# Kernel tuning notes

Hardware: AMD Instinct MI355X
Metric: run time of the kernel (lower is better)

## Reference

```python
import jax, jax.numpy as jnp
import numpy as np

DT = 1e-4  # integration step, matches Model(dt=0.0001)
T = 4_000_000


def setup_inputs() -> dict:
    key = jax.random.key(0)
    ks = jax.random.split(key, 8)
    inputs = jax.random.normal(ks[0], (1, T, 3), dtype=jnp.float32)
    # time column made increasing (as in a real signal record)
    t = jnp.arange(T, dtype=jnp.float32) * DT
    inputs = inputs.at[0, :, 0].set(t)
    # small-scale 2x2 system matrices; A shifted toward -0.5*I so the
    # 4M-step linear recurrence is stable (no overflow over long horizons)
    A = -0.5 * jnp.eye(2, dtype=jnp.float32) + 0.05 * jax.random.normal(ks[1], (2, 2), jnp.float32)
    B = 0.1 * jax.random.normal(ks[2], (2, 2), jnp.float32)
    D = 0.1 * jax.random.normal(ks[3], (2, 2), jnp.float32)
    E = 0.1 * jax.random.normal(ks[4], (2, 2), jnp.float32)
    cov_in = 0.1 * jax.random.normal(ks[5], (2, 2), jnp.float32)
    training_params = jax.random.normal(ks[6], (1, 2), jnp.float32)
    initial_states = jnp.zeros((1, 5), dtype=jnp.float32)
    return {"inputs": inputs, "A": A, "B": B, "D": D, "E": E,
            "cov_in": cov_in, "training_params": training_params,
            "initial_states": initial_states}


def reference(inputs, A, B, D, E, cov_in, training_params, initial_states):
    # Faithful to GRCell.call: cov = cov_in every step (new_cov is discarded),
    # so XiCov / XiCovC / transition matrix are time-invariant constants.
    dt = jnp.float32(DT)
    sqrt2 = jnp.sqrt(jnp.float32(2.0))
    x_signal = jnp.array([1.0, 0.0], dtype=inputs.dtype)
    XiCov = (E - cov_in @ B) / sqrt2                      # (2,2)
    XiCovC = XiCov @ (-sqrt2 * B.T)                       # (2,2)
    Trans = jnp.eye(2, dtype=inputs.dtype) + (A - XiCovC) * dt  # I + (A-XiCovC)dt
    Cout = -sqrt2 * B.T * dt                              # output map, (2,2)
    p0 = training_params[0, 0]
    p1 = training_params[0, 1]
    seq = inputs[0]                                       # [T, 3] = (time, dy1, dy2)

    def step(x, inp):
        t = inp[0]
        dy = inp[1:]
        out = Cout @ x                                    # emitted BEFORE update
        x_new = Trans @ x + XiCov @ dy + (p0 * jnp.cos(p1 * t) * dt) * x_signal
        return x_new, out

    x0 = initial_states[0, :2]
    _, outs = jax.lax.scan(step, x0, seq)                 # outs: [T, 2]
    return outs[None]                                     # [1, T, 2]
```

## Files before the change

kernel.cpp:

```cpp
#include <hip/hip_runtime.h>
#include <math.h>


constexpr int   TN    = 4000000;
constexpr float FDT   = 1e-4f;
constexpr int   L     = 16;
constexpr int   LOG2L = 4;
constexpr int   K     = TN / L;
constexpr int   BT    = 256;
constexpr int   NB    = (K + BT - 1) / BT;
constexpr int   ROW   = 13;
constexpr int   F4IN  = TN * 3 / 4;
constexpr int   F4OUT = TN * 2 / 4;

struct Consts {
  float T00, T01, T10, T11;
  float X00, X01, X10, X11;
  float C00, C01, C10, C11;
  float p0, p1;
};

__device__ inline Consts make_consts(const float* __restrict__ A,
                                     const float* __restrict__ B,
                                     const float* __restrict__ E,
                                     const float* __restrict__ cov,
                                     const float* __restrict__ tp) {
  const float s2 = 1.41421356237309515f;
  Consts c;
  float Xi[2][2];
  for (int i = 0; i < 2; ++i)
    for (int j = 0; j < 2; ++j)
      Xi[i][j] = (E[i*2+j] - (cov[i*2+0]*B[0*2+j] + cov[i*2+1]*B[1*2+j])) / s2;
  float XiC[2][2];
  for (int i = 0; i < 2; ++i)
    for (int j = 0; j < 2; ++j)
      XiC[i][j] = Xi[i][0]*(-s2*B[j*2+0]) + Xi[i][1]*(-s2*B[j*2+1]);
  c.T00 = 1.0f + (A[0] - XiC[0][0]) * FDT;
  c.T01 =        (A[1] - XiC[0][1]) * FDT;
  c.T10 =        (A[2] - XiC[1][0]) * FDT;
  c.T11 = 1.0f + (A[3] - XiC[1][1]) * FDT;
  c.X00 = Xi[0][0]; c.X01 = Xi[0][1]; c.X10 = Xi[1][0]; c.X11 = Xi[1][1];
  c.C00 = -s2 * B[0] * FDT;
  c.C01 = -s2 * B[2] * FDT;
  c.C10 = -s2 * B[1] * FDT;
  c.C11 = -s2 * B[3] * FDT;
  c.p0 = tp[0]; c.p1 = tp[1];
  return c;
}

__device__ inline void step(float& x0, float& x1, float t, float a, float b,
                            const Consts& c) {
  float u0 = fmaf(c.X00, a, fmaf(c.X01, b, c.p0 * __cosf(c.p1 * t) * FDT));
  float u1 = fmaf(c.X10, a, c.X11 * b);
  float n0 = fmaf(c.T00, x0, fmaf(c.T01, x1, u0));
  float n1 = fmaf(c.T10, x0, fmaf(c.T11, x1, u1));
  x0 = n0; x1 = n1;
}

__device__ inline void dsq(double* M) {
  double a = M[0]*M[0] + M[1]*M[2];
  double b = M[0]*M[1] + M[1]*M[3];
  double d = M[2]*M[0] + M[3]*M[2];
  double e = M[2]*M[1] + M[3]*M[3];
  M[0] = a; M[1] = b; M[2] = d; M[3] = e;
}

__device__ inline void dmm(const double* a, const double* b, double* o) {
  o[0] = a[0]*b[0] + a[1]*b[2];
  o[1] = a[0]*b[1] + a[1]*b[3];
  o[2] = a[2]*b[0] + a[3]*b[2];
  o[3] = a[2]*b[1] + a[3]*b[3];
}

__device__ inline void pow_table(const Consts& c, double (*Pw)[4], int n) {
  double M[4] = {(double)c.T00, (double)c.T01, (double)c.T10, (double)c.T11};
  for (int s = 0; s < LOG2L; ++s) dsq(M);
  Pw[0][0] = M[0]; Pw[0][1] = M[1]; Pw[0][2] = M[2]; Pw[0][3] = M[3];
  for (int i = 1; i < n; ++i) {
    dsq(M);
    Pw[i][0] = M[0]; Pw[i][1] = M[1]; Pw[i][2] = M[2]; Pw[i][3] = M[3];
  }
}

__global__ void __launch_bounds__(BT)
k1(const float* __restrict__ seq, const float* __restrict__ A,
   const float* __restrict__ B, const float* __restrict__ E,
   const float* __restrict__ cov, const float* __restrict__ tp,
   float2* __restrict__ Xe, double2* __restrict__ agg) {
  __shared__ float4  ls[BT * ROW];
  __shared__ double  wg[4][2];
  const int tid  = threadIdx.x;
  const int lane = tid & 63;
  const int w    = tid >> 6;
  const int k    = blockIdx.x * BT + tid;
  Consts c = make_consts(A, B, E, cov, tp);

  const float4* seq4 = (const float4*)seq;
  const size_t base = (size_t)blockIdx.x * (BT * 12);
  #pragma unroll
  for (int i = 0; i < 12; ++i) {
    int lf = i * BT + tid;
    size_t f = base + (size_t)lf;
    float4 v = make_float4(0.f, 0.f, 0.f, 0.f);
    if (f < (size_t)F4IN) v = seq4[f];
    int cc = lf / 12, s = lf - cc * 12;
    ls[cc * ROW + s] = v;
  }
  __syncthreads();

  float x0 = 0.f, x1 = 0.f;
  const float4* row = &ls[tid * ROW];
  #pragma unroll
  for (int q = 0; q < 4; ++q) {
    float4 fa = row[3*q], fb = row[3*q+1], fc = row[3*q+2];
    step(x0, x1, fa.x, fa.y, fa.z, c);
    step(x0, x1, fa.w, fb.x, fb.y, c);
    step(x0, x1, fb.z, fb.w, fc.x, c);
    step(x0, x1, fc.y, fc.z, fc.w, c);
  }

  double Pw[7][4];
  pow_table(c, Pw, 7);

  double v0 = (double)x0, v1 = (double)x1;
  #pragma unroll
  for (int s = 0; s < 6; ++s) {
    int st = 1 << s;
    double p0 = __shfl_up(v0, st);
    double p1 = __shfl_up(v1, st);
    if (lane >= st) {
      double n0 = Pw[s][0]*p0 + Pw[s][1]*p1 + v0;
      double n1 = Pw[s][2]*p0 + Pw[s][3]*p1 + v1;
      v0 = n0; v1 = n1;
    }
  }
  if (lane == 63) { wg[w][0] = v0; wg[w][1] = v1; }
  __syncthreads();

  double E0 = 0.0, E1 = 0.0;
  for (int ww = 0; ww < w; ++ww) {
    double n0 = Pw[6][0]*E0 + Pw[6][1]*E1 + wg[ww][0];
    double n1 = Pw[6][2]*E0 + Pw[6][3]*E1 + wg[ww][1];
    E0 = n0; E1 = n1;
  }

  double pv0 = __shfl_up(v0, 1);
  double pv1 = __shfl_up(v1, 1);
  if (lane == 0) { pv0 = 0.0; pv1 = 0.0; }

  double M0 = 1.0, M1 = 0.0, M2 = 0.0, M3 = 1.0;
  #pragma unroll
  for (int b = 0; b < 6; ++b) {
    if ((lane >> b) & 1) {
      double a0 = Pw[b][0]*M0 + Pw[b][1]*M2;
      double a1 = Pw[b][0]*M1 + Pw[b][1]*M3;
      double a2 = Pw[b][2]*M0 + Pw[b][3]*M2;
      double a3 = Pw[b][2]*M1 + Pw[b][3]*M3;
      M0 = a0; M1 = a1; M2 = a2; M3 = a3;
    }
  }
  double e0 = M0*E0 + M1*E1 + pv0;
  double e1 = M2*E0 + M3*E1 + pv1;
  if (k < K) Xe[k] = make_float2((float)e0, (float)e1);
  if (tid == BT - 1) {
    double a0 = Pw[6][0]*E0 + Pw[6][1]*E1 + v0;
    double a1 = Pw[6][2]*E0 + Pw[6][3]*E1 + v1;
    agg[blockIdx.x] = make_double2(a0, a1);
  }
}

__global__ void __launch_bounds__(BT)
k2(const float* __restrict__ A, const float* __restrict__ B,
   const float* __restrict__ E, const float* __restrict__ cov,
   const float* __restrict__ tp, const float* __restrict__ ini,
   const double2* __restrict__ agg, double2* __restrict__ Yb) {
  __shared__ double wg[4][2];
  const int tid = threadIdx.x, lane = tid & 63, w = tid >> 6;
  Consts c = make_consts(A, B, E, cov, tp);

  double Q[4] = {(double)c.T00, (double)c.T01, (double)c.T10, (double)c.T11};
  for (int s = 0; s < LOG2L + 8; ++s) dsq(Q);
  double Q2[4], Q3[4], Q4[4];
  dmm(Q, Q, Q2); dmm(Q2, Q, Q3); dmm(Q2, Q2, Q4);
  double QW[7][4];
  for (int i = 0; i < 4; ++i) QW[0][i] = Q4[i];
  for (int s = 1; s < 7; ++s) dmm(QW[s-1], QW[s-1], QW[s]);

  double i0 = 0.0, i1 = 0.0;
  double inc[4][2];
  #pragma unroll
  for (int j = 0; j < 4; ++j) {
    int idx = 4 * tid + j;
    double e0 = 0.0, e1 = 0.0;
    if (idx == 0)      { e0 = (double)ini[0]; e1 = (double)ini[1]; }
    else if (idx < NB) { double2 a = agg[idx-1]; e0 = a.x; e1 = a.y; }
    double n0 = Q[0]*i0 + Q[1]*i1 + e0;
    double n1 = Q[2]*i0 + Q[3]*i1 + e1;
    i0 = n0; i1 = n1;
    inc[j][0] = i0; inc[j][1] = i1;
  }

  double v0 = i0, v1 = i1;
  #pragma unroll
  for (int s = 0; s < 6; ++s) {
    int st = 1 << s;
    double p0 = __shfl_up(v0, st);
    double p1 = __shfl_up(v1, st);
    if (lane >= st) {
      double n0 = QW[s][0]*p0 + QW[s][1]*p1 + v0;
      double n1 = QW[s][2]*p0 + QW[s][3]*p1 + v1;
      v0 = n0; v1 = n1;
    }
  }
  if (lane == 63) { wg[w][0] = v0; wg[w][1] = v1; }
  __syncthreads();
  double E0 = 0.0, E1 = 0.0;
  for (int ww = 0; ww < w; ++ww) {
    double n0 = QW[6][0]*E0 + QW[6][1]*E1 + wg[ww][0];
    double n1 = QW[6][2]*E0 + QW[6][3]*E1 + wg[ww][1];
    E0 = n0; E1 = n1;
  }
  double pv0 = __shfl_up(v0, 1);
  double pv1 = __shfl_up(v1, 1);
  if (lane == 0) { pv0 = 0.0; pv1 = 0.0; }

  double M0 = 1.0, M1 = 0.0, M2 = 0.0, M3 = 1.0;
  #pragma unroll
  for (int b = 0; b < 6; ++b) {
    if ((lane >> b) & 1) {
      double a0 = QW[b][0]*M0 + QW[b][1]*M2;
      double a1 = QW[b][0]*M1 + QW[b][1]*M3;
      double a2 = QW[b][2]*M0 + QW[b][3]*M2;
      double a3 = QW[b][2]*M1 + QW[b][3]*M3;
      M0 = a0; M1 = a1; M2 = a2; M3 = a3;
    }
  }
  double Eth0 = M0*E0 + M1*E1 + pv0;
  double Eth1 = M2*E0 + M3*E1 + pv1;

  const double* Pj[4] = {Q, Q2, Q3, Q4};
  #pragma unroll
  for (int j = 0; j < 4; ++j) {
    int idx = 4 * tid + j;
    if (idx < NB) {
      double y0 = Pj[j][0]*Eth0 + Pj[j][1]*Eth1 + inc[j][0];
      double y1 = Pj[j][2]*Eth0 + Pj[j][3]*Eth1 + inc[j][1];
      Yb[idx] = make_double2(y0, y1);
    }
  }
}

__global__ void __launch_bounds__(BT)
k3(const float* __restrict__ seq, const float* __restrict__ A,
   const float* __restrict__ B, const float* __restrict__ E,
   const float* __restrict__ cov, const float* __restrict__ tp,
   const float2* __restrict__ Xe, const double2* __restrict__ Yb,
   float* __restrict__ out) {
  __shared__ float4 ls[BT * ROW];
  const int tid = threadIdx.x;
  const int k   = blockIdx.x * BT + tid;
  Consts c = make_consts(A, B, E, cov, tp);

  const float4* seq4 = (const float4*)seq;
  const size_t base = (size_t)blockIdx.x * (BT * 12);
  #pragma unroll
  for (int i = 0; i < 12; ++i) {
    int lf = i * BT + tid;
    size_t f = base + (size_t)lf;
    float4 v = make_float4(0.f, 0.f, 0.f, 0.f);
    if (f < (size_t)F4IN) v = seq4[f];
    int cc = lf / 12, s = lf - cc * 12;
    ls[cc * ROW + s] = v;
  }
  __syncthreads();

  double Pw[8][4];
  pow_table(c, Pw, 8);
  double M0 = 1.0, M1 = 0.0, M2 = 0.0, M3 = 1.0;
  #pragma unroll
  for (int b = 0; b < 8; ++b) {
    if ((tid >> b) & 1) {
      double a0 = Pw[b][0]*M0 + Pw[b][1]*M2;
      double a1 = Pw[b][0]*M1 + Pw[b][1]*M3;
      double a2 = Pw[b][2]*M0 + Pw[b][3]*M2;
      double a3 = Pw[b][2]*M1 + Pw[b][3]*M3;
      M0 = a0; M1 = a1; M2 = a2; M3 = a3;
    }
  }
  double2 yb = Yb[blockIdx.x];
  float2 xe = (k < K) ? Xe[k] : make_float2(0.f, 0.f);
  float x0 = (float)(M0*yb.x + M1*yb.y + (double)xe.x);
  float x1 = (float)(M2*yb.x + M3*yb.y + (double)xe.y);

  float4* row = &ls[tid * ROW];
  #pragma unroll
  for (int q = 0; q < 4; ++q) {
    float4 fa = row[3*q], fb = row[3*q+1], fc = row[3*q+2];
    float4 oA, oB;
    oA.x = fmaf(c.C00, x0, c.C01 * x1); oA.y = fmaf(c.C10, x0, c.C11 * x1);
    step(x0, x1, fa.x, fa.y, fa.z, c);
    oA.z = fmaf(c.C00, x0, c.C01 * x1); oA.w = fmaf(c.C10, x0, c.C11 * x1);
    step(x0, x1, fa.w, fb.x, fb.y, c);
    oB.x = fmaf(c.C00, x0, c.C01 * x1); oB.y = fmaf(c.C10, x0, c.C11 * x1);
    step(x0, x1, fb.z, fb.w, fc.x, c);
    oB.z = fmaf(c.C00, x0, c.C01 * x1); oB.w = fmaf(c.C10, x0, c.C11 * x1);
    step(x0, x1, fc.y, fc.z, fc.w, c);
    row[2*q]   = oA;
    row[2*q+1] = oB;
  }
  __syncthreads();

  float4* out4 = (float4*)out;
  const size_t obase = (size_t)blockIdx.x * (BT * 8);
  #pragma unroll
  for (int i = 0; i < 8; ++i) {
    int lf = i * BT + tid;
    size_t g = obase + (size_t)lf;
    if (g < (size_t)F4OUT) {
      int cc = lf >> 3, s = lf & 7;
      out4[g] = ls[cc * ROW + s];
    }
  }
}

extern "C" void kernel_launch(void* const* d_in, const int* in_sizes, int n_in,
                              void* d_out, int out_size, void* d_ws, size_t ws_size,
                              hipStream_t stream) {
  const float* seq = (const float*)d_in[0];
  const float* A   = (const float*)d_in[1];
  const float* B   = (const float*)d_in[2];
  const float* E   = (const float*)d_in[4];
  const float* cov = (const float*)d_in[5];
  const float* tp  = (const float*)d_in[6];
  const float* ini = (const float*)d_in[7];
  float* out = (float*)d_out;

  float2*  Xe  = (float2*)d_ws;
  double2* agg = (double2*)((char*)d_ws + 2000000);
  double2* Yb  = (double2*)((char*)d_ws + 2000000 + 16384);

  k1<<<NB, BT, 0, stream>>>(seq, A, B, E, cov, tp, Xe, agg);
  k2<<<1,  BT, 0, stream>>>(A, B, E, cov, tp, ini, agg, Yb);
  k3<<<NB, BT, 0, stream>>>(seq, A, B, E, cov, tp, Xe, Yb, out);
}
```

Baseline: 127.0 us.

## Fuse three scan kernels into one persistent kernel with grid barrier

The three launches (local scan, block-carry scan, fixup) become one persistent kernel of 512 blocks, each handling up to two tiles. An atomic grid barrier separates the phases, and every block redundantly computes the cross-block carry scan. Per-thread carries stay in registers, so the Xe/Yb workspace round trips and two launch gaps go away. The cost is a spin barrier that assumes all 512 blocks are co-resident, a memset launch, and reloading the inputs from global memory in the second phase.

Result: slower. 356.5 us (+180.8%).

```diff
diff --git a/kernel.cpp b/kernel.cpp
--- a/kernel.cpp
+++ b/kernel.cpp
@@ -8,7 +8,8 @@
 constexpr int   LOG2L = 4;
 constexpr int   K     = TN / L;
 constexpr int   BT    = 256;
-constexpr int   NB    = (K + BT - 1) / BT;
+constexpr int   NT    = (K + BT - 1) / BT;
+constexpr int   NBLK  = 512;
 constexpr int   ROW   = 13;
 constexpr int   F4IN  = TN * 3 / 4;
 constexpr int   F4OUT = TN * 2 / 4;
@@ -72,114 +73,127 @@
   o[3] = a[2]*b[1] + a[3]*b[3];
 }
 
-__device__ inline void pow_table(const Consts& c, double (*Pw)[4], int n) {
+__device__ inline void mulleft(const double* P, double* M) {
+  double a0 = P[0]*M[0] + P[1]*M[2];
+  double a1 = P[0]*M[1] + P[1]*M[3];
+  double a2 = P[2]*M[0] + P[3]*M[2];
+  double a3 = P[2]*M[1] + P[3]*M[3];
+  M[0]=a0; M[1]=a1; M[2]=a2; M[3]=a3;
+}
+
+__device__ inline void pow_table(const Consts& c, double (*Pt)[4], int n) {
   double M[4] = {(double)c.T00, (double)c.T01, (double)c.T10, (double)c.T11};
   for (int s = 0; s < LOG2L; ++s) dsq(M);
-  Pw[0][0] = M[0]; Pw[0][1] = M[1]; Pw[0][2] = M[2]; Pw[0][3] = M[3];
+  Pt[0][0] = M[0]; Pt[0][1] = M[1]; Pt[0][2] = M[2]; Pt[0][3] = M[3];
   for (int i = 1; i < n; ++i) {
     dsq(M);
-    Pw[i][0] = M[0]; Pw[i][1] = M[1]; Pw[i][2] = M[2]; Pw[i][3] = M[3];
-  }
-}
-
-__global__ void __launch_bounds__(BT)
-k1(const float* __restrict__ seq, const float* __restrict__ A,
-   const float* __restrict__ B, const float* __restrict__ E,
-   const float* __restrict__ cov, const float* __restrict__ tp,
-   float2* __restrict__ Xe, double2* __restrict__ agg) {
-  __shared__ float4  ls[BT * ROW];
-  __shared__ double  wg[4][2];
+    Pt[i][0] = M[0]; Pt[i][1] = M[1]; Pt[i][2] = M[2]; Pt[i][3] = M[3];
+  }
+}
+
+__global__ void __launch_bounds__(BT, 2)
+fused(const float* __restrict__ seq, const float* __restrict__ A,
+      const float* __restrict__ B, const float* __restrict__ Em,
+      const float* __restrict__ cov, const float* __restrict__ tp,
+      const float* __restrict__ ini,
+      int* __restrict__ bar, double* __restrict__ agg,
+      float* __restrict__ out) {
+  __shared__ float4 ls[BT * ROW];
+  __shared__ double wg[4][2];
+  __shared__ double sY[2][2];
   const int tid  = threadIdx.x;
   const int lane = tid & 63;
   const int w    = tid >> 6;
-  const int k    = blockIdx.x * BT + tid;
-  Consts c = make_consts(A, B, E, cov, tp);
+  const int bid  = blockIdx.x;
+  Consts c = make_consts(A, B, Em, cov, tp);
+
+  double Pt[8][4];
+  pow_table(c, Pt, 8);
+
+  double Mt[4] = {1,0,0,1};
+  #pragma unroll
+  for (int b = 0; b < 8; ++b) if ((tid >> b) & 1) mulleft(Pt[b], Mt);
+  double Ml[4] = {1,0,0,1};
+  #pragma unroll
+  for (int b = 0; b < 6; ++b) if ((lane >> b) & 1) mulleft(Pt[b], Ml);
 
   const float4* seq4 = (const float4*)seq;
-  const size_t base = (size_t)blockIdx.x * (BT * 12);
-  #pragma unroll
-  for (int i = 0; i < 12; ++i) {
-    int lf = i * BT + tid;
-    size_t f = base + (size_t)lf;
-    float4 v = make_float4(0.f, 0.f, 0.f, 0.f);
-    if (f < (size_t)F4IN) v = seq4[f];
-    int cc = lf / 12, s = lf - cc * 12;
-    ls[cc * ROW + s] = v;
-  }
+  double xe[2][2];
+
+  for (int tt = 0; tt < 2; ++tt) {
+    int t = bid + tt * NBLK;
+    if (t >= NT) break;
+    if (tt) __syncthreads();
+    const size_t base = (size_t)t * (BT * 12);
+    #pragma unroll
+    for (int i = 0; i < 12; ++i) {
+      int lf = i * BT + tid;
+      size_t f = base + (size_t)lf;
+      float4 v = make_float4(0.f, 0.f, 0.f, 0.f);
+      if (f < (size_t)F4IN) v = seq4[f];
+      int cc = lf / 12, s = lf - cc * 12;
+      ls[cc * ROW + s] = v;
+    }
+    __syncthreads();
+
+    float x0 = 0.f, x1 = 0.f;
+    const float4* row = &ls[tid * ROW];
+    #pragma unroll
+    for (int q = 0; q < 4; ++q) {
+      float4 fa = row[3*q], fb = row[3*q+1], fc = row[3*q+2];
+      step(x0, x1, fa.x, fa.y, fa.z, c);
+      step(x0, x1, fa.w, fb.x, fb.y, c);
+      step(x0, x1, fb.z, fb.w, fc.x, c);
+      step(x0, x1, fc.y, fc.z, fc.w, c);
+    }
+
+    double v0 = (double)x0, v1 = (double)x1;
+    #pragma unroll
+    for (int s = 0; s < 6; ++s) {
+      int st = 1 << s;
+      double p0 = __shfl_up(v0, st);
+      double p1 = __shfl_up(v1, st);
+      if (lane >= st) {
+        double n0 = Pt[s][0]*p0 + Pt[s][1]*p1 + v0;
+        double n1 = Pt[s][2]*p0 + Pt[s][3]*p1 + v1;
+        v0 = n0; v1 = n1;
+      }
+    }
+    if (lane == 63) { wg[w][0] = v0; wg[w][1] = v1; }
+    __syncthreads();
+    double E0 = 0.0, E1 = 0.0;
+    for (int ww = 0; ww < w; ++ww) {
+      double n0 = Pt[6][0]*E0 + Pt[6][1]*E1 + wg[ww][0];
+      double n1 = Pt[6][2]*E0 + Pt[6][3]*E1 + wg[ww][1];
+      E0 = n0; E1 = n1;
+    }
+    double pv0 = __shfl_up(v0, 1);
+    double pv1 = __shfl_up(v1, 1);
+    if (lane == 0) { pv0 = 0.0; pv1 = 0.0; }
+    xe[tt][0] = Ml[0]*E0 + Ml[1]*E1 + pv0;
+    xe[tt][1] = Ml[2]*E0 + Ml[3]*E1 + pv1;
+    if (tid == BT - 1) {
+      double a0 = Pt[6][0]*E0 + Pt[6][1]*E1 + v0;
+      double a1 = Pt[6][2]*E0 + Pt[6][3]*E1 + v1;
+      __hip_atomic_store(&agg[2*t],   a0, __ATOMIC_RELEASE, __HIP_MEMORY_SCOPE_AGENT);
+      __hip_atomic_store(&agg[2*t+1], a1, __ATOMIC_RELEASE, __HIP_MEMORY_SCOPE_AGENT);
+    }
+  }
+
+  __threadfence();
   __syncthreads();
-
-  float x0 = 0.f, x1 = 0.f;
-  const float4* row = &ls[tid * ROW];
-  #pragma unroll
-  for (int q = 0; q < 4; ++q) {
-    float4 fa = row[3*q], fb = row[3*q+1], fc = row[3*q+2];
-    step(x0, x1, fa.x, fa.y, fa.z, c);
-    step(x0, x1, fa.w, fb.x, fb.y, c);
-    step(x0, x1, fb.z, fb.w, fc.x, c);
-    step(x0, x1, fc.y, fc.z, fc.w, c);
-  }
-
-  double Pw[7][4];
-  pow_table(c, Pw, 7);
-
-  double v0 = (double)x0, v1 = (double)x1;
-  #pragma unroll
-  for (int s = 0; s < 6; ++s) {
-    int st = 1 << s;
-    double p0 = __shfl_up(v0, st);
-    double p1 = __shfl_up(v1, st);
-    if (lane >= st) {
-      double n0 = Pw[s][0]*p0 + Pw[s][1]*p1 + v0;
-      double n1 = Pw[s][2]*p0 + Pw[s][3]*p1 + v1;
-      v0 = n0; v1 = n1;
-    }
-  }
-  if (lane == 63) { wg[w][0] = v0; wg[w][1] = v1; }
+  if (tid == 0) {
+    __hip_atomic_fetch_add(bar, 1, __ATOMIC_ACQ_REL, __HIP_MEMORY_SCOPE_AGENT);
+    long guard = 0;
+    while (__hip_atomic_load(bar, __ATOMIC_ACQUIRE, __HIP_MEMORY_SCOPE_AGENT) < NBLK) {
+      __builtin_amdgcn_s_sleep(2);
+      if (++guard > (1L << 26)) break;
+    }
+  }
   __syncthreads();
 
-  double E0 = 0.0, E1 = 0.0;
-  for (int ww = 0; ww < w; ++ww) {
-    double n0 = Pw[6][0]*E0 + Pw[6][1]*E1 + wg[ww][0];
-    double n1 = Pw[6][2]*E0 + Pw[6][3]*E1 + wg[ww][1];
-    E0 = n0; E1 = n1;
-  }
-
-  double pv0 = __shfl_up(v0, 1);
-  double pv1 = __shfl_up(v1, 1);
-  if (lane == 0) { pv0 = 0.0; pv1 = 0.0; }
-
-  double M0 = 1.0, M1 = 0.0, M2 = 0.0, M3 = 1.0;
-  #pragma unroll
-  for (int b = 0; b < 6; ++b) {
-    if ((lane >> b) & 1) {
-      double a0 = Pw[b][0]*M0 + Pw[b][1]*M2;
-      double a1 = Pw[b][0]*M1 + Pw[b][1]*M3;
-      double a2 = Pw[b][2]*M0 + Pw[b][3]*M2;
-      double a3 = Pw[b][2]*M1 + Pw[b][3]*M3;
-      M0 = a0; M1 = a1; M2 = a2; M3 = a3;
-    }
-  }
-  double e0 = M0*E0 + M1*E1 + pv0;
-  double e1 = M2*E0 + M3*E1 + pv1;
-  if (k < K) Xe[k] = make_float2((float)e0, (float)e1);
-  if (tid == BT - 1) {
-    double a0 = Pw[6][0]*E0 + Pw[6][1]*E1 + v0;
-    double a1 = Pw[6][2]*E0 + Pw[6][3]*E1 + v1;
-    agg[blockIdx.x] = make_double2(a0, a1);
-  }
-}
-
-__global__ void __launch_bounds__(BT)
-k2(const float* __restrict__ A, const float* __restrict__ B,
-   const float* __restrict__ E, const float* __restrict__ cov,
-   const float* __restrict__ tp, const float* __restrict__ ini,
-   const double2* __restrict__ agg, double2* __restrict__ Yb) {
-  __shared__ double wg[4][2];
-  const int tid = threadIdx.x, lane = tid & 63, w = tid >> 6;
-  Consts c = make_consts(A, B, E, cov, tp);
-
-  double Q[4] = {(double)c.T00, (double)c.T01, (double)c.T10, (double)c.T11};
-  for (int s = 0; s < LOG2L + 8; ++s) dsq(Q);
+  double Q[4] = {Pt[7][0], Pt[7][1], Pt[7][2], Pt[7][3]};
+  dsq(Q);
   double Q2[4], Q3[4], Q4[4];
   dmm(Q, Q, Q2); dmm(Q2, Q, Q3); dmm(Q2, Q2, Q4);
   double QW[7][4];
@@ -192,14 +206,16 @@
   for (int j = 0; j < 4; ++j) {
     int idx = 4 * tid + j;
     double e0 = 0.0, e1 = 0.0;
-    if (idx == 0)      { e0 = (double)ini[0]; e1 = (double)ini[1]; }
-    else if (idx < NB) { double2 a = agg[idx-1]; e0 = a.x; e1 = a.y; }
+    if (idx == 0) { e0 = (double)ini[0]; e1 = (double)ini[1]; }
+    else if (idx < NT) {
+      e0 = __hip_atomic_load(&agg[2*(idx-1)],   __ATOMIC_ACQUIRE, __HIP_MEMORY_SCOPE_AGENT);
+      e1 = __hip_atomic_load(&agg[2*(idx-1)+1], __ATOMIC_ACQUIRE, __HIP_MEMORY_SCOPE_AGENT);
+    }
     double n0 = Q[0]*i0 + Q[1]*i1 + e0;
     double n1 = Q[2]*i0 + Q[3]*i1 + e1;
     i0 = n0; i1 = n1;
     inc[j][0] = i0; inc[j][1] = i1;
   }
-
   double v0 = i0, v1 = i1;
   #pragma unroll
   for (int s = 0; s < 6; ++s) {
@@ -223,7 +239,6 @@
   double pv0 = __shfl_up(v0, 1);
   double pv1 = __shfl_up(v1, 1);
   if (lane == 0) { pv0 = 0.0; pv1 = 0.0; }
-
   double M0 = 1.0, M1 = 0.0, M2 = 0.0, M3 = 1.0;
   #pragma unroll
   for (int b = 0; b < 6; ++b) {
@@ -238,87 +253,66 @@
   double Eth0 = M0*E0 + M1*E1 + pv0;
   double Eth1 = M2*E0 + M3*E1 + pv1;
 
-  const double* Pj[4] = {Q, Q2, Q3, Q4};
-  #pragma unroll
-  for (int j = 0; j < 4; ++j) {
-    int idx = 4 * tid + j;
-    if (idx < NB) {
+  {
+    const double* Pj[4] = {Q, Q2, Q3, Q4};
+    #pragma unroll
+    for (int j = 0; j < 4; ++j) {
+      int idx = 4 * tid + j;
       double y0 = Pj[j][0]*Eth0 + Pj[j][1]*Eth1 + inc[j][0];
       double y1 = Pj[j][2]*Eth0 + Pj[j][3]*Eth1 + inc[j][1];
-      Yb[idx] = make_double2(y0, y1);
-    }
-  }
-}
-
-__global__ void __launch_bounds__(BT)
-k3(const float* __restrict__ seq, const float* __restrict__ A,
-   const float* __restrict__ B, const float* __restrict__ E,
-   const float* __restrict__ cov, const float* __restrict__ tp,
-   const float2* __restrict__ Xe, const double2* __restrict__ Yb,
-   float* __restrict__ out) {
-  __shared__ float4 ls[BT * ROW];
-  const int tid = threadIdx.x;
-  const int k   = blockIdx.x * BT + tid;
-  Consts c = make_consts(A, B, E, cov, tp);
-
-  const float4* seq4 = (const float4*)seq;
-  const size_t base = (size_t)blockIdx.x * (BT * 12);
-  #pragma unroll
-  for (int i = 0; i < 12; ++i) {
-    int lf = i * BT + tid;
-    size_t f = base + (size_t)lf;
-    float4 v = make_float4(0.f, 0.f, 0.f, 0.f);
-    if (f < (size_t)F4IN) v = seq4[f];
-    int cc = lf / 12, s = lf - cc * 12;
-    ls[cc * ROW + s] = v;
-  }
-  __syncthreads();
-
-  double Pw[8][4];
-  pow_table(c, Pw, 8);
-  double M0 = 1.0, M1 = 0.0, M2 = 0.0, M3 = 1.0;
-  #pragma unroll
-  for (int b = 0; b < 8; ++b) {
-    if ((tid >> b) & 1) {
-      double a0 = Pw[b][0]*M0 + Pw[b][1]*M2;
-      double a1 = Pw[b][0]*M1 + Pw[b][1]*M3;
-      double a2 = Pw[b][2]*M0 + Pw[b][3]*M2;
-      double a3 = Pw[b][2]*M1 + Pw[b][3]*M3;
-      M0 = a0; M1 = a1; M2 = a2; M3 = a3;
-    }
-  }
-  double2 yb = Yb[blockIdx.x];
-  float2 xe = (k < K) ? Xe[k] : make_float2(0.f, 0.f);
-  float x0 = (float)(M0*yb.x + M1*yb.y + (double)xe.x);
-  float x1 = (float)(M2*yb.x + M3*yb.y + (double)xe.y);
-
-  float4* row = &ls[tid * ROW];
-  #pragma unroll
-  for (int q = 0; q < 4; ++q) {
-    float4 fa = row[3*q], fb = row[3*q+1], fc = row[3*q+2];
-    float4 oA, oB;
-    oA.x = fmaf(c.C00, x0, c.C01 * x1); oA.y = fmaf(c.C10, x0, c.C11 * x1);
-    step(x0, x1, fa.x, fa.y, fa.z, c);
-    oA.z = fmaf(c.C00, x0, c.C01 * x1); oA.w = fmaf(c.C10, x0, c.C11 * x1);
-    step(x0, x1, fa.w, fb.x, fb.y, c);
-    oB.x = fmaf(c.C00, x0, c.C01 * x1); oB.y = fmaf(c.C10, x0, c.C11 * x1);
-    step(x0, x1, fb.z, fb.w, fc.x, c);
-    oB.z = fmaf(c.C00, x0, c.C01 * x1); oB.w = fmaf(c.C10, x0, c.C11 * x1);
-    step(x0, x1, fc.y, fc.z, fc.w, c);
-    row[2*q]   = oA;
-    row[2*q+1] = oB;
-  }
-  __syncthreads();
-
-  float4* out4 = (float4*)out;
-  const size_t obase = (size_t)blockIdx.x * (BT * 8);
-  #pragma unroll
-  for (int i = 0; i < 8; ++i) {
-    int lf = i * BT + tid;
-    size_t g = obase + (size_t)lf;
-    if (g < (size_t)F4OUT) {
-      int cc = lf >> 3, s = lf & 7;
-      out4[g] = ls[cc * ROW + s];
+      if (idx == bid)                      { sY[0][0] = y0; sY[0][1] = y1; }
+      if (idx == bid + NBLK && idx < NT)   { sY[1][0] = y0; sY[1][1] = y1; }
+    }
+  }
+
+  for (int tt = 0; tt < 2; ++tt) {
+    int t = bid + tt * NBLK;
+    if (t >= NT) break;
+    __syncthreads();
+    const size_t base = (size_t)t * (BT * 12);
+    #pragma unroll
+    for (int i = 0; i < 12; ++i) {
+      int lf = i * BT + tid;
+      size_t f = base + (size_t)lf;
+      float4 v = make_float4(0.f, 0.f, 0.f, 0.f);
+      if (f < (size_t)F4IN) v = seq4[f];
+      int cc = lf / 12, s = lf - cc * 12;
+      ls[cc * ROW + s] = v;
+    }
+    __syncthreads();
+
+    double y0 = sY[tt][0], y1 = sY[tt][1];
+    float x0 = (float)(Mt[0]*y0 + Mt[1]*y1 + xe[tt][0]);
+    float x1 = (float)(Mt[2]*y0 + Mt[3]*y1 + xe[tt][1]);
+
+    float4* row = &ls[tid * ROW];
+    #pragma unroll
+    for (int q = 0; q < 4; ++q) {
+      float4 fa = row[3*q], fb = row[3*q+1], fc = row[3*q+2];
+      float4 oA, oB;
+      oA.x = fmaf(c.C00, x0, c.C01 * x1); oA.y = fmaf(c.C10, x0, c.C11 * x1);
+      step(x0, x1, fa.x, fa.y, fa.z, c);
+      oA.z = fmaf(c.C00, x0, c.C01 * x1); oA.w = fmaf(c.C10, x0, c.C11 * x1);
+      step(x0, x1, fa.w, fb.x, fb.y, c);
+      oB.x = fmaf(c.C00, x0, c.C01 * x1); oB.y = fmaf(c.C10, x0, c.C11 * x1);
+      step(x0, x1, fb.z, fb.w, fc.x, c);
+      oB.z = fmaf(c.C00, x0, c.C01 * x1); oB.w = fmaf(c.C10, x0, c.C11 * x1);
+      step(x0, x1, fc.y, fc.z, fc.w, c);
+      row[2*q]   = oA;
+      row[2*q+1] = oB;
+    }
+    __syncthreads();
+
+    float4* out4 = (float4*)out;
+    const size_t obase = (size_t)t * (BT * 8);
+    #pragma unroll
+    for (int i = 0; i < 8; ++i) {
+      int lf = i * BT + tid;
+      size_t g = obase + (size_t)lf;
+      if (g < (size_t)F4OUT) {
+        int cc = lf >> 3, s = lf & 7;
+        out4[g] = ls[cc * ROW + s];
+      }
     }
   }
 }
@@ -335,11 +329,9 @@
   const float* ini = (const float*)d_in[7];
   float* out = (float*)d_out;
 
-  float2*  Xe  = (float2*)d_ws;
-  double2* agg = (double2*)((char*)d_ws + 2000000);
-  double2* Yb  = (double2*)((char*)d_ws + 2000000 + 16384);
-
-  k1<<<NB, BT, 0, stream>>>(seq, A, B, E, cov, tp, Xe, agg);
-  k2<<<1,  BT, 0, stream>>>(A, B, E, cov, tp, ini, agg, Yb);
-  k3<<<NB, BT, 0, stream>>>(seq, A, B, E, cov, tp, Xe, Yb, out);
-}
+  int*    bar = (int*)d_ws;
+  double* agg = (double*)((char*)d_ws + 256);
+
+  hipMemsetAsync(d_ws, 0, 256, stream);
+  fused<<<NBLK, BT, 0, stream>>>(seq, A, B, E, cov, tp, ini, bar, agg, out);
+}
```
